# Kernel tuning notes

Measured on AMD Instinct MI355X. Metric: run time of the kernel, lower is better.

Reference implementation:

```python
import jax, jax.numpy as jnp
import numpy as np
from jax.scipy.special import logsumexp

SINKHORN_ITERS = 3
EPS = 1e-12


def setup_inputs() -> dict:
    key = jax.random.key(0)
    ks = jax.random.split(key, 10)
    B, C, H, W = 32, 384, 48, 48
    HID, D, K = 512, 128, 64
    s = 0.05
    return {
        "x": jax.random.normal(ks[0], (B, C, H, W), dtype=jnp.float32),
        # cluster_features branch: 1x1 convs == per-pixel matmuls
        "w1": jax.random.normal(ks[1], (HID, C), dtype=jnp.float32) * s,
        "b1": jax.random.normal(ks[2], (HID,), dtype=jnp.float32) * s,
        "w2": jax.random.normal(ks[3], (D, HID), dtype=jnp.float32) * s,
        "b2": jax.random.normal(ks[4], (D,), dtype=jnp.float32) * s,
        # score branch
        "s1": jax.random.normal(ks[5], (HID, C), dtype=jnp.float32) * s,
        "c1": jax.random.normal(ks[6], (HID,), dtype=jnp.float32) * s,
        "s2": jax.random.normal(ks[7], (K, HID), dtype=jnp.float32) * s,
        "c2": jax.random.normal(ks[8], (K,), dtype=jnp.float32) * s,
        "alpha": jnp.asarray(1.0, dtype=jnp.float32),  # dust_bin
    }


def _log_optimal_transport(scores, alpha, iters):
    # scores: [b, m, n] with m = num_clusters, n = num tokens
    b, m, n = scores.shape
    norm = -jnp.log(jnp.asarray(m + n, dtype=scores.dtype))
    bins = jnp.broadcast_to(alpha, (b, 1, n)).astype(scores.dtype)
    Z = jnp.concatenate([scores, bins], axis=1)  # [b, m+1, n]
    log_mu = jnp.concatenate([
        jnp.full((m,), norm, dtype=scores.dtype),
        jnp.log(jnp.asarray(n - m, dtype=scores.dtype))[None] + norm,
    ])  # [m+1]
    log_nu = jnp.full((n,), norm, dtype=scores.dtype)
    log_mu = jnp.broadcast_to(log_mu, (b, m + 1))
    log_nu = jnp.broadcast_to(log_nu, (b, n))

    u = jnp.zeros_like(log_mu)
    v = jnp.zeros_like(log_nu)
    for _ in range(iters):
        u = log_mu - logsumexp(Z + v[:, None, :], axis=2)
        v = log_nu - logsumexp(Z + u[:, :, None], axis=1)
    return Z + u[:, :, None] + v[:, None, :] - norm


def reference(x, w1, b1, w2, b2, s1, c1, s2, c2, alpha):
    B, C, H, W = x.shape
    xf = x.reshape(B, C, H * W)  # [b, c, n]
    # cluster features: 1x1 conv -> relu -> 1x1 conv (dropout is identity in eval)
    h = jnp.maximum(jnp.einsum('oc,bcn->bon', w1, xf) + b1[:, None], 0.0)
    f = jnp.einsum('oc,bcn->bon', w2, h) + b2[:, None]  # [b, D, n]
    # scores
    hs = jnp.maximum(jnp.einsum('oc,bcn->bon', s1, xf) + c1[:, None], 0.0)
    p = jnp.einsum('oc,bcn->bon', s2, hs) + c2[:, None]  # [b, K, n]
    # log-domain optimal transport with dust bin
    Z = _log_optimal_transport(p, alpha, SINKHORN_ITERS)
    P = jnp.exp(Z)[:, :-1, :]  # [b, K, n], drop dust bin row
    # repeat-mul-sum pooling == batched contraction over tokens
    agg = jnp.einsum('bdn,bkn->bdk', f, P)  # [b, D, K]
    nrm = jnp.sqrt(jnp.sum(agg * agg, axis=1, keepdims=True))
    agg = agg / jnp.maximum(nrm, EPS)  # L2 normalize over cluster_dim
    return agg.reshape(B, -1)  # [b, D*K]
```

## Files before the change

### kernel.cpp

```cpp
#include <hip/hip_runtime.h>
#include <math.h>
#include <stdint.h>

#define HW_N 2304
#define CB   384
#define HIDD 512
#define HID2 1024
#define DD   128
#define KK   64
#define BATCH 32
#define M1   65
#define NTOK (BATCH * HW_N)
#define NORM_ARG 2368.0f

typedef __bf16 bf16;
typedef __bf16 bf16x8 __attribute__((ext_vector_type(8)));
typedef float  f32x4  __attribute__((ext_vector_type(4)));

__device__ __forceinline__ void gld16(void* lds, const void* g) {
    __builtin_amdgcn_global_load_lds(
        (const __attribute__((address_space(1))) uint32_t*)g,
        (__attribute__((address_space(3))) uint32_t*)lds, 16, 0, 0);
}

template<int N> __device__ __forceinline__ void waitvm() {
    if constexpr (N == 0)  asm volatile("s_waitcnt vmcnt(0)"  ::: "memory");
    else if constexpr (N == 1)  asm volatile("s_waitcnt vmcnt(1)"  ::: "memory");
    else if constexpr (N == 2)  asm volatile("s_waitcnt vmcnt(2)"  ::: "memory");
    else if constexpr (N == 3)  asm volatile("s_waitcnt vmcnt(3)"  ::: "memory");
    else if constexpr (N == 4)  asm volatile("s_waitcnt vmcnt(4)"  ::: "memory");
    else if constexpr (N == 5)  asm volatile("s_waitcnt vmcnt(5)"  ::: "memory");
    else if constexpr (N == 6)  asm volatile("s_waitcnt vmcnt(6)"  ::: "memory");
    else if constexpr (N == 7)  asm volatile("s_waitcnt vmcnt(7)"  ::: "memory");
    else if constexpr (N == 8)  asm volatile("s_waitcnt vmcnt(8)"  ::: "memory");
    else if constexpr (N == 9)  asm volatile("s_waitcnt vmcnt(9)"  ::: "memory");
    else if constexpr (N == 10) asm volatile("s_waitcnt vmcnt(10)" ::: "memory");
    else if constexpr (N == 11) asm volatile("s_waitcnt vmcnt(11)" ::: "memory");
    else if constexpr (N == 12) asm volatile("s_waitcnt vmcnt(12)" ::: "memory");
    else asm volatile("s_waitcnt vmcnt(0)" ::: "memory");
}

__global__ __launch_bounds__(256)
void x_to_bf16T(const float* __restrict__ x, bf16* __restrict__ xT)
{
    const int b  = blockIdx.z;
    const int n0 = blockIdx.x * 64;
    const int c0 = blockIdx.y * 64;
    __shared__ float t[64][65];
    const int tx = threadIdx.x & 15, ty = threadIdx.x >> 4;
    const float* xb = x + (long)b * CB * HW_N;
    #pragma unroll
    for (int r = 0; r < 64; r += 16) {
        const float4 vv = *(const float4*)&xb[(long)(c0 + r + ty) * HW_N + n0 + tx * 4];
        t[r + ty][tx * 4 + 0] = vv.x; t[r + ty][tx * 4 + 1] = vv.y;
        t[r + ty][tx * 4 + 2] = vv.z; t[r + ty][tx * 4 + 3] = vv.w;
    }
    __syncthreads();
    bf16* ob = xT + (long)b * HW_N * CB;
    #pragma unroll
    for (int r = 0; r < 64; r += 16) {
        const int n = r + ty;
        union { bf16 h[4]; uint2 u2; } pk;
        pk.h[0] = (bf16)t[tx * 4 + 0][n]; pk.h[1] = (bf16)t[tx * 4 + 1][n];
        pk.h[2] = (bf16)t[tx * 4 + 2][n]; pk.h[3] = (bf16)t[tx * 4 + 3][n];
        *(uint2*)&ob[(long)(n0 + n) * CB + c0 + tx * 4] = pk.u2;
    }
}

__device__ __forceinline__ void cvtq(const float* __restrict__ in,
                                     bf16* __restrict__ out, int q)
{
    float4 vv = ((const float4*)in)[q];
    union { bf16 h[4]; uint2 u2; } pk;
    pk.h[0] = (bf16)vv.x; pk.h[1] = (bf16)vv.y;
    pk.h[2] = (bf16)vv.z; pk.h[3] = (bf16)vv.w;
    ((uint2*)out)[q] = pk.u2;
}

__global__ __launch_bounds__(256)
void prep_weights(const float* __restrict__ w1, const float* __restrict__ s1,
                  const float* __restrict__ w2, const float* __restrict__ s2,
                  const float* __restrict__ b1, const float* __restrict__ c1,
                  bf16* __restrict__ Wc, bf16* __restrict__ Wf,
                  float* __restrict__ bc)
{
    const int QW1 = HIDD * CB / 4;
    const int QW2 = DD * HIDD / 4;
    const int QS2 = KK * HIDD / 4;
    int i = blockIdx.x * 256 + threadIdx.x;
    if (i < QW1)                       { cvtq(w1, Wc, i); return; }
    i -= QW1;
    if (i < QW1)                       { cvtq(s1, Wc + (long)HIDD * CB, i); return; }
    i -= QW1;
    if (i < QW2)                       { cvtq(w2, Wf, i); return; }
    i -= QW2;
    if (i < QS2)                       { cvtq(s2, Wf + (long)DD * HIDD, i); return; }
    i -= QS2;
    if (i < 256) {
        float4 vv = (i < 128) ? ((const float4*)b1)[i] : ((const float4*)c1)[i - 128];
        ((float4*)bc)[i] = vv;
    }
}

template<int FA, int FB, int OUT_MODE, bool RELU, int MINW>
__global__ __launch_bounds__(256, MINW)
void mfma_gemm4(const bf16* __restrict__ A, int lda,
                const bf16* __restrict__ B, int ldb,
                const float* __restrict__ bias,
                void* __restrict__ OUT, int ldo,
                int K, int nA)
{
    constexpr int BA = 2 * FA * 16;
    constexpr int BB = 2 * FB * 16;
    constexpr int ROWB = 64;
    constexpr int GA = (BA * ROWB) / 4096;
    constexpr int GB = (BB * ROWB) / 4096;
    constexpr int GAB = GA + GB;

    __shared__ __align__(16) bf16 As[3][BA * 32];
    __shared__ __align__(16) bf16 Bs[3][BB * 32];

    int L = blockIdx.x;
    { const int cpx = gridDim.x >> 3; L = (L & 7) * cpx + (L >> 3); }
    const int ta = L % nA;
    const int tb = L / nA;

    const int tid  = threadIdx.x;
    const int lane = tid & 63;
    const int w    = tid >> 6;
    const int wr   = w >> 1, wc = w & 1;

    const char* Ap = (const char*)A + (long)ta * BA * lda * 2;
    const char* Bp = (const char*)B + (long)tb * BB * ldb * 2;
    const long ldab = (long)lda * 2, ldbb = (long)ldb * 2;

    const int subrow = lane >> 2;
    const int colb   = (lane & 3) << 4;
    const int rl = lane & 15, q = lane >> 4;

    f32x4 acc[FA][FB];
    #pragma unroll
    for (int i = 0; i < FA; i++)
        #pragma unroll
        for (int j = 0; j < FB; j++)
            acc[i][j] = (f32x4){0.f, 0.f, 0.f, 0.f};

    const int nsteps = K / 32;

    auto stageA = [&](int buf, int kt) {
        #pragma unroll
        for (int g = 0; g < GA; ++g) {
            const int ii = g * 4 + w;
            gld16((char*)As[buf] + ii * 1024,
                  Ap + (long)(ii * 16 + subrow) * ldab + (long)kt * ROWB + colb);
        }
    };
    auto stageB = [&](int buf, int kt) {
        #pragma unroll
        for (int g = 0; g < GB; ++g) {
            const int ii = g * 4 + w;
            gld16((char*)Bs[buf] + ii * 1024,
                  Bp + (long)(ii * 16 + subrow) * ldbb + (long)kt * ROWB + colb);
        }
    };

    stageA(0, 0); stageB(0, 0);
    if (nsteps > 1) { stageA(1, 1); stageB(1, 1); }
    if (nsteps > 2) { stageA(2, 2); stageB(2, 2); }
    if (nsteps > 2)      waitvm<2 * GAB>();
    else if (nsteps > 1) waitvm<GAB>();
    else                 waitvm<0>();
    __builtin_amdgcn_s_barrier();

    for (int t = 0; t < nsteps; ++t) {
        const int cur = t % 3;
        const char* Ab = (const char*)As[cur];
        const char* Bb = (const char*)Bs[cur];

        bf16x8 a[FA], bb[FB];
        #pragma unroll
        for (int i = 0; i < FA; i++)
            a[i] = *(const bf16x8*)(Ab + (wr * FA * 16 + i * 16 + rl) * ROWB + (q << 4));
        #pragma unroll
        for (int j = 0; j < FB; j++)
            bb[j] = *(const bf16x8*)(Bb + (wc * FB * 16 + j * 16 + rl) * ROWB + (q << 4));

        __builtin_amdgcn_s_setprio(1);
        #pragma unroll
        for (int i = 0; i < FA; i++)
            #pragma unroll
            for (int j = 0; j < FB; j++)
                acc[i][j] = __builtin_amdgcn_mfma_f32_16x16x32_bf16(a[i], bb[j], acc[i][j], 0, 0, 0);
        __builtin_amdgcn_s_setprio(0);

        asm volatile("s_waitcnt lgkmcnt(0)" ::: "memory");
        __builtin_amdgcn_s_barrier();
        if (t + 3 < nsteps) { stageA(cur, t + 3); stageB(cur, t + 3); }
        if (t + 1 < nsteps) {
            if (t + 3 < nsteps)      waitvm<2 * GAB>();
            else if (t + 2 < nsteps) waitvm<GAB>();
            else                     waitvm<0>();
            __builtin_amdgcn_s_barrier();
        }
    }

    const int fr = lane & 15;
    const int fq = lane >> 4;

    if (OUT_MODE == 0) {
        #pragma unroll
        for (int i = 0; i < FA; i++) {
            const int ra0 = ta * BA + wr * FA * 16 + i * 16 + fq * 4;
            const float4 bv = *(const float4*)&bias[ra0];
            #pragma unroll
            for (int j = 0; j < FB; j++) {
                const int rb = tb * BB + wc * FB * 16 + j * 16 + fr;
                union { bf16 h[4]; uint2 u2; } pk;
                float v0 = acc[i][j][0] + bv.x, v1 = acc[i][j][1] + bv.y;
                float v2 = acc[i][j][2] + bv.z, v3 = acc[i][j][3] + bv.w;
                if (RELU) {
                    v0 = fmaxf(v0, 0.f); v1 = fmaxf(v1, 0.f);
                    v2 = fmaxf(v2, 0.f); v3 = fmaxf(v3, 0.f);
                }
                pk.h[0] = (bf16)v0; pk.h[1] = (bf16)v1;
                pk.h[2] = (bf16)v2; pk.h[3] = (bf16)v3;
                *(uint2*)&((bf16*)OUT)[(long)rb * ldo + ra0] = pk.u2;
            }
        }
    } else {
        #pragma unroll
        for (int i = 0; i < FA; i++) {
            const int g0 = ta * BA + wr * FA * 16 + i * 16 + fq * 4;
            const int bi = g0 / HW_N;
            const int nn = g0 - bi * HW_N;
            #pragma unroll
            for (int j = 0; j < FB; j++) {
                const int mg = tb * BB + wc * FB * 16 + j * 16 + fr;
                const float bvs = bias[mg];
                float v0 = acc[i][j][0] + bvs, v1 = acc[i][j][1] + bvs;
                float v2 = acc[i][j][2] + bvs, v3 = acc[i][j][3] + bvs;
                if (RELU) {
                    v0 = fmaxf(v0, 0.f); v1 = fmaxf(v1, 0.f);
                    v2 = fmaxf(v2, 0.f); v3 = fmaxf(v3, 0.f);
                }
                const long base = ((long)bi * ldo + mg) * HW_N + nn;
                if (OUT_MODE == 1) {
                    union { bf16 h[4]; uint2 u2; } pk;
                    pk.h[0] = (bf16)v0; pk.h[1] = (bf16)v1;
                    pk.h[2] = (bf16)v2; pk.h[3] = (bf16)v3;
                    *(uint2*)&((bf16*)OUT)[base] = pk.u2;
                } else {
                    *(float4*)&((float*)OUT)[base] = make_float4(v0, v1, v2, v3);
                }
            }
        }
    }
}

template<bool FIRST>
__global__ __launch_bounds__(256)
void sink_u(const float* __restrict__ Z, const float* __restrict__ v,
            const float* __restrict__ alpha, float* __restrict__ u)
{
    const int b = blockIdx.y;
    const int i = blockIdx.x * 4 + (threadIdx.x >> 6);
    if (i > KK) return;
    const int lane = threadIdx.x & 63;
    const float* zr = Z + ((long)b * KK + i) * HW_N;
    const float* vb = v + (long)b * HW_N;
    const float a = alpha[0];
    float m = -INFINITY, s = 0.f;
    for (int j = lane; j < HW_N; j += 64) {
        float val = (i < KK) ? zr[j] : a;
        if (!FIRST) val += vb[j];
        float mn = fmaxf(m, val);
        s = s * __expf(m - mn) + __expf(val - mn);
        m = mn;
    }
    #pragma unroll
    for (int off = 32; off; off >>= 1) {
        float m2 = __shfl_xor(m, off), s2 = __shfl_xor(s, off);
        float mn = fmaxf(m, m2);
        s = s * __expf(m - mn) + s2 * __expf(m2 - mn);
        m = mn;
    }
    if (lane == 0) {
        const float norm = -logf(NORM_ARG);
        const float logmu = (i < KK) ? norm : (logf((float)(HW_N - KK)) + norm);
        u[b * M1 + i] = logmu - (m + __logf(s));
    }
}

__global__ __launch_bounds__(256)
void sink_v(const float* __restrict__ Z, const float* __restrict__ u,
            const float* __restrict__ alpha, float* __restrict__ v)
{
    const int b = blockIdx.y;
    const int n = blockIdx.x * 256 + threadIdx.x;
    const float* ub = u + b * M1;
    const float* Zb = Z + (long)b * KK * HW_N;
    float m = alpha[0] + ub[KK];
    float s = 1.f;
    for (int i = 0; i < KK; i++) {
        float t = Zb[(long)i * HW_N + n] + ub[i];
        float mn = fmaxf(m, t);
        s = s * __expf(m - mn) + __expf(t - mn);
        m = mn;
    }
    const float norm = -logf(NORM_ARG);
    v[(long)b * HW_N + n] = norm - (m + __logf(s));
}

__global__ __launch_bounds__(256)
void agg_partial(const bf16* __restrict__ f, const float* __restrict__ Z,
                 const float* __restrict__ u, const float* __restrict__ v,
                 float* __restrict__ part)
{
    const int c = blockIdx.x;
    const int b = blockIdx.y;
    const int n0 = c << 8;
    const float norm = -logf(NORM_ARG);

    __shared__ float Fs[16][132];
    __shared__ float Ps[16][68];

    const bf16*  fb = f + (long)b * DD * HW_N;
    const float* Zb = Z + (long)b * KK * HW_N;
    const float* ub = u + b * M1;
    const float* vb = v + (long)b * HW_N;

    const int tid = threadIdx.x;
    const int td = tid & 31;
    const int tk = tid >> 5;

    const int fd = tid >> 1, fh = tid & 1;
    const int pk_ = tid >> 2, pq = tid & 3;

    float acc[4][8] = {};

    for (int nt = 0; nt < 256; nt += 16) {
        {
            union { uint4 u4; unsigned short s[8]; } pv;
            pv.u4 = *(const uint4*)&fb[(long)fd * HW_N + n0 + nt + fh * 8];
            #pragma unroll
            for (int r = 0; r < 8; r++) {
                union { uint32_t q; float fv; } cv;
                cv.q = (uint32_t)pv.s[r] << 16;
                Fs[fh * 8 + r][fd] = cv.fv;
            }
        }
        {
            const int n = n0 + nt + pq * 4;
            const float4 z = *(const float4*)&Zb[(long)pk_ * HW_N + n];
            const float uk = ub[pk_];
            Ps[pq * 4 + 0][pk_] = __expf(z.x + uk + vb[n + 0] - norm);
            Ps[pq * 4 + 1][pk_] = __expf(z.y + uk + vb[n + 1] - norm);
            Ps[pq * 4 + 2][pk_] = __expf(z.z + uk + vb[n + 2] - norm);
            Ps[pq * 4 + 3][pk_] = __expf(z.w + uk + vb[n + 3] - norm);
        }
        __syncthreads();
        #pragma unroll
        for (int nn = 0; nn < 16; nn++) {
            const float4 av = *reinterpret_cast<const float4*>(&Fs[nn][td << 2]);
            const float4 p0 = *reinterpret_cast<const float4*>(&Ps[nn][tk << 3]);
            const float4 p1 = *reinterpret_cast<const float4*>(&Ps[nn][(tk << 3) + 4]);
            float a[4] = {av.x, av.y, av.z, av.w};
            float p[8] = {p0.x, p0.y, p0.z, p0.w, p1.x, p1.y, p1.z, p1.w};
            #pragma unroll
            for (int i = 0; i < 4; i++)
                #pragma unroll
                for (int j = 0; j < 8; j++)
                    acc[i][j] += a[i] * p[j];
        }
        __syncthreads();
    }

    float* pb = part + (long)(b * 9 + c) * (DD * KK);
    #pragma unroll
    for (int i = 0; i < 4; i++) {
        int d = (td << 2) + i;
        float4 o0 = make_float4(acc[i][0], acc[i][1], acc[i][2], acc[i][3]);
        float4 o1 = make_float4(acc[i][4], acc[i][5], acc[i][6], acc[i][7]);
        *reinterpret_cast<float4*>(&pb[d * KK + (tk << 3)]) = o0;
        *reinterpret_cast<float4*>(&pb[d * KK + (tk << 3) + 4]) = o1;
    }
}

__global__ __launch_bounds__(256)
void finalize(const float* __restrict__ part, float* __restrict__ out)
{
    const int b = blockIdx.x;
    __shared__ float agg[DD * KK];
    __shared__ float nrm[KK];
    const int tid = threadIdx.x;

    for (int idx = tid; idx < DD * KK; idx += 256) {
        float s = 0.f;
        #pragma unroll
        for (int cc = 0; cc < 9; cc++)
            s += part[(long)(b * 9 + cc) * (DD * KK) + idx];
        agg[idx] = s;
    }
    __syncthreads();
    if (tid < KK) {
        float ss = 0.f;
        for (int d = 0; d < DD; d++) { float t = agg[d * KK + tid]; ss += t * t; }
        nrm[tid] = fmaxf(sqrtf(ss), 1e-12f);
    }
    __syncthreads();
    for (int idx = tid; idx < DD * KK; idx += 256)
        out[(long)b * (DD * KK) + idx] = agg[idx] / nrm[idx & 63];
}

extern "C" void kernel_launch(void* const* d_in, const int* in_sizes, int n_in,
                              void* d_out, int out_size, void* d_ws, size_t ws_size,
                              hipStream_t stream)
{
    const float* x     = (const float*)d_in[0];
    const float* w1    = (const float*)d_in[1];
    const float* b1    = (const float*)d_in[2];
    const float* w2    = (const float*)d_in[3];
    const float* b2    = (const float*)d_in[4];
    const float* s1    = (const float*)d_in[5];
    const float* c1    = (const float*)d_in[6];
    const float* s2    = (const float*)d_in[7];
    const float* c2    = (const float*)d_in[8];
    const float* alpha = (const float*)d_in[9];
    float* out = (float*)d_out;

    char* p = (char*)d_ws;
    bf16* Wc  = (bf16*)p;  p += (long)HID2 * CB * 2;
    bf16* Wf  = (bf16*)p;  p += (long)(DD + KK) * HIDD * 2;
    float* bc = (float*)p; p += (long)HID2 * 4;
    bf16* xT  = (bf16*)p;  p += (long)NTOK * CB * 2;
    bf16* hs  = (bf16*)p;  p += (long)NTOK * HID2 * 2;
    bf16* f   = (bf16*)p;  p += (long)BATCH * DD * HW_N * 2;
    float* Z  = (float*)p; p += (long)BATCH * KK * HW_N * 4;
    float* u  = (float*)p; p += (long)BATCH * M1 * 4;
    float* v  = (float*)p; p += (long)BATCH * HW_N * 4;
    float* part = (float*)p;

    prep_weights<<<481, 256, 0, stream>>>(w1, s1, w2, s2, b1, c1, Wc, Wf, bc);

    x_to_bf16T<<<dim3(36, 6, 32), 256, 0, stream>>>(x, xT);

    mfma_gemm4<4, 4, 0, true, 3><<<4608, 256, 0, stream>>>(
        Wc, CB, xT, CB, bc, hs, HID2, CB, HID2 / 128);

    mfma_gemm4<4, 4, 1, false, 3><<<NTOK / 128, 256, 0, stream>>>(
        hs, HID2, Wf, HIDD, b2, f, DD, HIDD, NTOK / 128);

    mfma_gemm4<4, 2, 2, false, 3><<<NTOK / 128, 256, 0, stream>>>(
        hs + HIDD, HID2, Wf + (long)DD * HIDD, HIDD, c2, Z, KK, HIDD, NTOK / 128);

    sink_u<true ><<<dim3(17, 32), 256, 0, stream>>>(Z, v, alpha, u);
    sink_v<<<dim3(9, 32), 256, 0, stream>>>(Z, u, alpha, v);
    sink_u<false><<<dim3(17, 32), 256, 0, stream>>>(Z, v, alpha, u);
    sink_v<<<dim3(9, 32), 256, 0, stream>>>(Z, u, alpha, v);
    sink_u<false><<<dim3(17, 32), 256, 0, stream>>>(Z, v, alpha, u);
    sink_v<<<dim3(9, 32), 256, 0, stream>>>(Z, u, alpha, v);

    agg_partial<<<dim3(9, 32), 256, 0, stream>>>(f, Z, u, v, part);
    finalize<<<32, 256, 0, stream>>>(part, out);
}
```

Before: 301.0 us.

## Rework GEMM LDS pipelines: double-buffer second-stage GEMMs, single-barrier triple buffer for first

The generic GEMM kernel drops from three LDS stages to two, cutting shared memory per block, and the second-stage GEMMs raise their launch-bounds occupancy hint from 3 to 4 blocks per CU. The first GEMM moves to a new specialised kernel that keeps three buffers but prefetches two steps ahead before computing, so it needs only one barrier per K step instead of two. The aim is more resident blocks on the long-K GEMMs and less barrier stalling on the short-K first GEMM. In exchange, the two-stage pipeline has less latency hiding, and the higher occupancy target may increase register pressure.

```diff
diff --git a/kernel.cpp b/kernel.cpp
--- a/kernel.cpp
+++ b/kernel.cpp
@@ -33,10 +33,6 @@
     else if constexpr (N == 6)  asm volatile("s_waitcnt vmcnt(6)"  ::: "memory");
     else if constexpr (N == 7)  asm volatile("s_waitcnt vmcnt(7)"  ::: "memory");
     else if constexpr (N == 8)  asm volatile("s_waitcnt vmcnt(8)"  ::: "memory");
-    else if constexpr (N == 9)  asm volatile("s_waitcnt vmcnt(9)"  ::: "memory");
-    else if constexpr (N == 10) asm volatile("s_waitcnt vmcnt(10)" ::: "memory");
-    else if constexpr (N == 11) asm volatile("s_waitcnt vmcnt(11)" ::: "memory");
-    else if constexpr (N == 12) asm volatile("s_waitcnt vmcnt(12)" ::: "memory");
     else asm volatile("s_waitcnt vmcnt(0)" ::: "memory");
 }
 
@@ -117,8 +113,8 @@
     constexpr int GB = (BB * ROWB) / 4096;
     constexpr int GAB = GA + GB;
 
-    __shared__ __align__(16) bf16 As[3][BA * 32];
-    __shared__ __align__(16) bf16 Bs[3][BB * 32];
+    __shared__ __align__(16) bf16 As[2][BA * 32];
+    __shared__ __align__(16) bf16 Bs[2][BB * 32];
 
     int L = blockIdx.x;
     { const int cpx = gridDim.x >> 3; L = (L & 7) * cpx + (L >> 3); }
@@ -165,15 +161,12 @@
     };
 
     stageA(0, 0); stageB(0, 0);
-    if (nsteps > 1) { stageA(1, 1); stageB(1, 1); }
-    if (nsteps > 2) { stageA(2, 2); stageB(2, 2); }
-    if (nsteps > 2)      waitvm<2 * GAB>();
-    else if (nsteps > 1) waitvm<GAB>();
-    else                 waitvm<0>();
+    stageA(1, 1); stageB(1, 1);
+    waitvm<GAB>();
     __builtin_amdgcn_s_barrier();
 
     for (int t = 0; t < nsteps; ++t) {
-        const int cur = t % 3;
+        const int cur = t & 1;
         const char* Ab = (const char*)As[cur];
         const char* Bb = (const char*)Bs[cur];
 
@@ -195,11 +188,9 @@
 
         asm volatile("s_waitcnt lgkmcnt(0)" ::: "memory");
         __builtin_amdgcn_s_barrier();
-        if (t + 3 < nsteps) { stageA(cur, t + 3); stageB(cur, t + 3); }
+        if (t + 2 < nsteps) { stageA(cur, t + 2); stageB(cur, t + 2); }
         if (t + 1 < nsteps) {
-            if (t + 3 < nsteps)      waitvm<2 * GAB>();
-            else if (t + 2 < nsteps) waitvm<GAB>();
-            else                     waitvm<0>();
+            if (t + 2 < nsteps) waitvm<GAB>(); else waitvm<0>();
             __builtin_amdgcn_s_barrier();
         }
     }
@@ -257,6 +248,128 @@
     }
 }
 
+template<int FA, int FB, bool RELU, int MINW>
+__global__ __launch_bounds__(256, MINW)
+void mfma_gemm4_sb3(const bf16* __restrict__ A, int lda,
+                    const bf16* __restrict__ B, int ldb,
+                    const float* __restrict__ bias,
+                    bf16* __restrict__ OUT, int ldo,
+                    int K, int nA)
+{
+    constexpr int BA = 2 * FA * 16;
+    constexpr int BB = 2 * FB * 16;
+    constexpr int ROWB = 64;
+    constexpr int GA = (BA * ROWB) / 4096;
+    constexpr int GB = (BB * ROWB) / 4096;
+    constexpr int GAB = GA + GB;
+
+    __shared__ __align__(16) bf16 As[3][BA * 32];
+    __shared__ __align__(16) bf16 Bs[3][BB * 32];
+
+    int L = blockIdx.x;
+    { const int cpx = gridDim.x >> 3; L = (L & 7) * cpx + (L >> 3); }
+    const int ta = L % nA;
+    const int tb = L / nA;
+
+    const int tid  = threadIdx.x;
+    const int lane = tid & 63;
+    const int w    = tid >> 6;
+    const int wr   = w >> 1, wc = w & 1;
+
+    const char* Ap = (const char*)A + (long)ta * BA * lda * 2;
+    const char* Bp = (const char*)B + (long)tb * BB * ldb * 2;
+    const long ldab = (long)lda * 2, ldbb = (long)ldb * 2;
+
+    const int subrow = lane >> 2;
+    const int colb   = (lane & 3) << 4;
+    const int rl = lane & 15, q = lane >> 4;
+
+    f32x4 acc[FA][FB];
+    #pragma unroll
+    for (int i = 0; i < FA; i++)
+        #pragma unroll
+        for (int j = 0; j < FB; j++)
+            acc[i][j] = (f32x4){0.f, 0.f, 0.f, 0.f};
+
+    const int nsteps = K / 32;
+
+    auto stageA = [&](int buf, int kt) {
+        #pragma unroll
+        for (int g = 0; g < GA; ++g) {
+            const int ii = g * 4 + w;
+            gld16((char*)As[buf] + ii * 1024,
+                  Ap + (long)(ii * 16 + subrow) * ldab + (long)kt * ROWB + colb);
+        }
+    };
+    auto stageB = [&](int buf, int kt) {
+        #pragma unroll
+        for (int g = 0; g < GB; ++g) {
+            const int ii = g * 4 + w;
+            gld16((char*)Bs[buf] + ii * 1024,
+                  Bp + (long)(ii * 16 + subrow) * ldbb + (long)kt * ROWB + colb);
+        }
+    };
+
+    stageA(0, 0); stageB(0, 0);
+    stageA(1, 1); stageB(1, 1);
+    waitvm<GAB>();
+    __builtin_amdgcn_s_barrier();
+
+    for (int t = 0; t < nsteps; ++t) {
+        const int cur = t % 3;
+        if (t + 2 < nsteps) {
+            const int nb = (t + 2) % 3;
+            stageA(nb, t + 2); stageB(nb, t + 2);
+        }
+
+        const char* Ab = (const char*)As[cur];
+        const char* Bb = (const char*)Bs[cur];
+        bf16x8 a[FA], bb[FB];
+        #pragma unroll
+        for (int i = 0; i < FA; i++)
+            a[i] = *(const bf16x8*)(Ab + (wr * FA * 16 + i * 16 + rl) * ROWB + (q << 4));
+        #pragma unroll
+        for (int j = 0; j < FB; j++)
+            bb[j] = *(const bf16x8*)(Bb + (wc * FB * 16 + j * 16 + rl) * ROWB + (q << 4));
+
+        __builtin_amdgcn_s_setprio(1);
+        #pragma unroll
+        for (int i = 0; i < FA; i++)
+            #pragma unroll
+            for (int j = 0; j < FB; j++)
+                acc[i][j] = __builtin_amdgcn_mfma_f32_16x16x32_bf16(a[i], bb[j], acc[i][j], 0, 0, 0);
+        __builtin_amdgcn_s_setprio(0);
+
+        asm volatile("s_waitcnt lgkmcnt(0)" ::: "memory");
+        if (t + 1 < nsteps) {
+            if (t + 2 < nsteps) waitvm<GAB>(); else waitvm<0>();
+            __builtin_amdgcn_s_barrier();
+        }
+    }
+
+    const int fr = lane & 15;
+    const int fq = lane >> 4;
+    #pragma unroll
+    for (int i = 0; i < FA; i++) {
+        const int ra0 = ta * BA + wr * FA * 16 + i * 16 + fq * 4;
+        const float4 bv = *(const float4*)&bias[ra0];
+        #pragma unroll
+        for (int j = 0; j < FB; j++) {
+            const int rb = tb * BB + wc * FB * 16 + j * 16 + fr;
+            float v0 = acc[i][j][0] + bv.x, v1 = acc[i][j][1] + bv.y;
+            float v2 = acc[i][j][2] + bv.z, v3 = acc[i][j][3] + bv.w;
+            if (RELU) {
+                v0 = fmaxf(v0, 0.f); v1 = fmaxf(v1, 0.f);
+                v2 = fmaxf(v2, 0.f); v3 = fmaxf(v3, 0.f);
+            }
+            union { bf16 h[4]; uint2 u2; } pk;
+            pk.h[0] = (bf16)v0; pk.h[1] = (bf16)v1;
+            pk.h[2] = (bf16)v2; pk.h[3] = (bf16)v3;
+            *(uint2*)&OUT[(long)rb * ldo + ra0] = pk.u2;
+        }
+    }
+}
+
 template<bool FIRST>
 __global__ __launch_bounds__(256)
 void sink_u(const float* __restrict__ Z, const float* __restrict__ v,
@@ -444,13 +557,13 @@
 
     x_to_bf16T<<<dim3(36, 6, 32), 256, 0, stream>>>(x, xT);
 
-    mfma_gemm4<4, 4, 0, true, 3><<<4608, 256, 0, stream>>>(
+    mfma_gemm4_sb3<4, 4, true, 3><<<4608, 256, 0, stream>>>(
         Wc, CB, xT, CB, bc, hs, HID2, CB, HID2 / 128);
 
-    mfma_gemm4<4, 4, 1, false, 3><<<NTOK / 128, 256, 0, stream>>>(
+    mfma_gemm4<4, 4, 1, false, 4><<<NTOK / 128, 256, 0, stream>>>(
         hs, HID2, Wf, HIDD, b2, f, DD, HIDD, NTOK / 128);
 
-    mfma_gemm4<4, 2, 2, false, 3><<<NTOK / 128, 256, 0, stream>>>(
+    mfma_gemm4<4, 2, 2, false, 4><<<NTOK / 128, 256, 0, stream>>>(
         hs + HIDD, HID2, Wf + (long)DD * HIDD, HIDD, c2, Z, KK, HIDD, NTOK / 128);
 
     sink_u<true ><<<dim3(17, 32), 256, 0, stream>>>(Z, v, alpha, u);
```

Result: no change. 301.0 us (-0.0%).
